# Performance work log

Hardware: AMD Instinct MI355X
Metric: run time of the kernel (lower is better)

## Reference

```python
import jax, jax.numpy as jnp
import numpy as np

N = 100_000      # nodes
E = 1_600_000    # edges (before self loops)
F_IN = 128       # dataset.num_node_features
H = 64           # hidden_channels
C = 10           # dataset.num_classes
B = 128          # graphs in batch
NEG_SLOPE = 0.2  # GATConv default


def setup_inputs() -> dict:
    key = jax.random.key(0)
    ks = jax.random.split(key, 16)
    s = 0.05
    x = jax.random.normal(ks[0], (N, F_IN), jnp.float32)
    edge_index = jax.random.randint(ks[1], (2, E), 0, N, dtype=jnp.int32).astype(jnp.int64)
    batch = jnp.sort(jax.random.randint(ks[2], (N,), 0, B, dtype=jnp.int32)).astype(jnp.int64)
    inp = {"x": x, "edge_index": edge_index, "batch": batch}
    # GATConv params: lin weight [out,in], att_src/att_dst [out], bias [out]
    dims = [(H, F_IN), (H, H), (H, H)]
    for i, (o, fi) in enumerate(dims, start=1):
        k = jax.random.split(ks[2 + i], 4)
        inp[f"W{i}"] = jax.random.normal(k[0], (o, fi), jnp.float32) * s
        inp[f"a_src{i}"] = jax.random.normal(k[1], (o,), jnp.float32) * s
        inp[f"a_dst{i}"] = jax.random.normal(k[2], (o,), jnp.float32) * s
        inp[f"b{i}"] = jax.random.normal(k[3], (o,), jnp.float32) * s
    inp["W_lin"] = jax.random.normal(ks[8], (C, H), jnp.float32) * s
    inp["b_lin"] = jax.random.normal(ks[9], (C,), jnp.float32) * s
    return inp


def gat_conv(x, src, dst, W, a_src, a_dst, b):
    # x: [N,Fin]; src/dst: [E+N] (self loops appended)
    h = x @ W.T                      # [N,H]
    e_src = h @ a_src                # [N] per-node src score
    e_dst = h @ a_dst                # [N] per-node dst score
    e = jax.nn.leaky_relu(e_src[src] + e_dst[dst], NEG_SLOPE)  # [E+N]
    # segment softmax over incoming edges of each dst node
    m = jax.ops.segment_max(e, dst, num_segments=N)
    ex = jnp.exp(e - m[dst])
    denom = jax.ops.segment_sum(ex, dst, num_segments=N)
    alpha = ex / denom[dst]          # [E+N]
    out = jax.ops.segment_sum(h[src] * alpha[:, None], dst, num_segments=N)
    return out + b


def reference(x, edge_index, batch, W1, a_src1, a_dst1, b1,
              W2, a_src2, a_dst2, b2, W3, a_src3, a_dst3, b3,
              W_lin, b_lin):
    loops = jnp.arange(N, dtype=edge_index.dtype)
    src = jnp.concatenate([edge_index[0], loops])
    dst = jnp.concatenate([edge_index[1], loops])
    h = jax.nn.relu(gat_conv(x, src, dst, W1, a_src1, a_dst1, b1))
    h = jax.nn.relu(gat_conv(h, src, dst, W2, a_src2, a_dst2, b2))
    h = gat_conv(h, src, dst, W3, a_src3, a_dst3, b3)
    # global mean pool over graphs
    sums = jax.ops.segment_sum(h, batch, num_segments=B)          # [B,H]
    cnt = jax.ops.segment_sum(jnp.ones((N,), h.dtype), batch, num_segments=B)
    pooled = sums / jnp.maximum(cnt, 1.0)[:, None]
    # dropout is identity in eval mode
    return pooled @ W_lin.T + b_lin   # [B,C]
```

## Files before the change

kernel.cpp:

```cpp
#include <hip/hip_runtime.h>
#include <hip/hip_bf16.h>

#define NN 100000
#define EE 1600000
#define ETOT 1700000
#define FIN1 128
#define HD 64
#define NC 10
#define NB 128
#define NEG 0.2f
#define LOG2E 1.44269504f

#define NBKT 196
#define BCAP 10240
#define BLKE 4096


static constexpr size_t OFF_HA   = 0;
static constexpr size_t OFF_HB   = (size_t)NN * HD;
static constexpr size_t OFF_ESA  = (size_t)NN * HD * 2;
static constexpr size_t OFF_EDA  = OFF_ESA + (size_t)NN * 4;
static constexpr size_t OFF_ESB  = OFF_EDA + (size_t)NN * 4;
static constexpr size_t OFF_EDB  = OFF_ESB + (size_t)NN * 4;
static constexpr size_t OFF_ROW  = OFF_EDB + (size_t)NN * 4;
static constexpr size_t OFF_CSR  = OFF_ROW + (size_t)(NN + 4) * 4;
static constexpr size_t OFF_GC   = OFF_CSR + (size_t)ETOT * 4;
static constexpr size_t OFF_POOL = OFF_GC + 1024;

typedef __attribute__((ext_vector_type(8))) short short8;
typedef __attribute__((ext_vector_type(4))) float floatx4;
typedef __attribute__((ext_vector_type(2))) float floatx2;

__device__ __forceinline__ unsigned short f2bf(float f) {
  unsigned u = __float_as_uint(f);
  if ((u & 0x7F800000u) == 0x7F800000u) return (unsigned short)(u >> 16);
  return (unsigned short)((u + 0x7FFFu + ((u >> 16) & 1u)) >> 16);
}
__device__ __forceinline__ unsigned pk2(float a, float b) {
  return (unsigned)f2bf(a) | ((unsigned)f2bf(b) << 16);
}

#if __has_builtin(__builtin_amdgcn_cvt_pk_fp8_f32) && __has_builtin(__builtin_amdgcn_cvt_pk_f32_fp8)
#define HW_FP8 1
#endif
__device__ __forceinline__ unsigned enc1_fp8(float f) {
  _Float16 hf = (_Float16)f;
  unsigned short b = __builtin_bit_cast(unsigned short, hf);
  unsigned s = ((unsigned)b >> 8) & 0x80u;
  int mag = b & 0x7fff;
  if (mag < 0x2380) return s;
  int r = mag + 0x3F + ((mag >> 7) & 1);
  int m = (r >> 7) - 64;
  if (m > 0x7E) m = 0x7E;
  return s | (unsigned)m;
}
__device__ __forceinline__ unsigned pack4_fp8(float a, float b, float c, float d) {
#ifdef HW_FP8
  int w = __builtin_amdgcn_cvt_pk_fp8_f32(a, b, 0, false);
  w = __builtin_amdgcn_cvt_pk_fp8_f32(c, d, w, true);
  return (unsigned)w;
#else
  return enc1_fp8(a) | (enc1_fp8(b) << 8) | (enc1_fp8(c) << 16) | (enc1_fp8(d) << 24);
#endif
}
__device__ __forceinline__ float dec1_fp8(unsigned byte) {
  unsigned short hb = (unsigned short)(((byte & 0x80u) << 8) | ((byte & 0x7fu) << 7));
  _Float16 hf = __builtin_bit_cast(_Float16, hb);
  return (float)hf * 256.0f;
}
template <bool HI>
__device__ __forceinline__ floatx2 unpk2_fp8(unsigned w) {
#ifdef HW_FP8
  return __builtin_amdgcn_cvt_pk_f32_fp8((int)w, HI);
#else
  unsigned s = HI ? (w >> 16) : w;
  floatx2 r; r.x = dec1_fp8(s & 0xffu); r.y = dec1_fp8((s >> 8) & 0xffu);
  return r;
#endif
}

__global__ __launch_bounds__(256) void bucketA_kernel(
    const int* __restrict__ EI, unsigned* __restrict__ bucketed,
    int* __restrict__ gcur) {
  __shared__ int cnt[NBKT];
  __shared__ int base[NBKT];
  const int t = threadIdx.x;
  const long long start = (long long)blockIdx.x * BLKE;
  unsigned pk[BLKE / 256];
  short bk[BLKE / 256];
  for (int i = t; i < NBKT; i += 256) cnt[i] = 0;
  __syncthreads();
#pragma unroll
  for (int j = 0; j < BLKE / 256; j++) {
    long long k = start + t + 256 * j;
    bk[j] = -1;
    if (k < ETOT) {
      int s, d;
      if (k < EE) { s = EI[k]; d = EI[(long long)EE + k]; }
      else        { s = d = (int)(k - EE); }
      int b = d >> 9;
      pk[j] = ((unsigned)s << 9) | (unsigned)(d & 511);
      bk[j] = (short)b;
      atomicAdd(&cnt[b], 1);
    }
  }
  __syncthreads();
  if (t < NBKT) {
    base[t] = (cnt[t] > 0) ? atomicAdd(&gcur[t], cnt[t]) : 0;
    cnt[t] = 0;
  }
  __syncthreads();
#pragma unroll
  for (int j = 0; j < BLKE / 256; j++) {
    if (bk[j] >= 0) {
      int b = bk[j];
      int pos = base[b] + atomicAdd(&cnt[b], 1);
      if (pos < BCAP) bucketed[(long long)b * BCAP + pos] = pk[j];
    }
  }
}

__global__ __launch_bounds__(256) void bucketB_kernel(
    const unsigned* __restrict__ bucketed, const int* __restrict__ gcur,
    int* __restrict__ rowptr, int* __restrict__ csr) {
  __shared__ int sc[256];
  __shared__ int hist[512];
  __shared__ int cur[512];
  __shared__ int ssum[256];
  const int t = threadIdx.x;
  const int b = blockIdx.x;
  int gv = (t < NBKT) ? gcur[t] : 0;
  sc[t] = gv;
  __syncthreads();
  for (int off = 1; off < 256; off <<= 1) {
    int add = (t >= off) ? sc[t - off] : 0;
    __syncthreads();
    sc[t] += add;
    __syncthreads();
  }
  const int cnt = gcur[b];
  const int base = sc[b] - cnt;
  if (b == 0 && t == 0) rowptr[NN] = ETOT;
  const unsigned* bp = bucketed + (long long)b * BCAP;
  hist[t] = 0; hist[t + 256] = 0;
  __syncthreads();
  for (int i = t; i < cnt; i += 256) atomicAdd(&hist[bp[i] & 511], 1);
  __syncthreads();
  int a0 = hist[2 * t], a1 = hist[2 * t + 1];
  int s = a0 + a1;
  ssum[t] = s;
  __syncthreads();
  for (int off = 1; off < 256; off <<= 1) {
    int add = (t >= off) ? ssum[t - off] : 0;
    __syncthreads();
    ssum[t] += add;
    __syncthreads();
  }
  int ex = ssum[t] - s;
  cur[2 * t] = ex;
  cur[2 * t + 1] = ex + a0;
  int gn = b * 512 + 2 * t;
  if (gn < NN) rowptr[gn] = base + ex;
  if (gn + 1 < NN) rowptr[gn + 1] = base + ex + a0;
  __syncthreads();
  for (int i = t; i < cnt; i += 256) {
    unsigned e = bp[i];
    int pos = atomicAdd(&cur[e & 511], 1);
    csr[base + pos] = (int)(e >> 9);
  }
}

__global__ __launch_bounds__(256) void gemm1_kernel(
    const float* __restrict__ X, const float* __restrict__ W,
    const float* __restrict__ As, const float* __restrict__ Ad,
    unsigned* __restrict__ hout, float* __restrict__ es, float* __restrict__ ed) {
  constexpr int K = FIN1, RW = K / 2;
  __shared__ unsigned Xw[64 * RW];
  __shared__ unsigned Ww[64 * RW];
  const int t = threadIdx.x;
  const int nodeBase = blockIdx.x * 64;

  for (int i4 = t * 4; i4 < 64 * K; i4 += 1024) {
    int node = i4 >> 7, k = i4 & (K - 1);
    float4 v = make_float4(0.f, 0.f, 0.f, 0.f);
    if (nodeBase + node < NN)
      v = *(const float4*)(X + ((long long)(nodeBase + node) << 7) + k);
    uint2 p = make_uint2(pk2(v.x, v.y), pk2(v.z, v.w));
    int kw = k >> 1;
    *(uint2*)&Xw[node * RW + (kw ^ ((node & 7) << 2))] = p;
  }
  for (int i4 = t * 4; i4 < 64 * K; i4 += 1024) {
    int f = i4 >> 7, k = i4 & (K - 1);
    float4 v = *(const float4*)(W + ((long long)f << 7) + k);
    uint2 p = make_uint2(pk2(v.x, v.y), pk2(v.z, v.w));
    int kw = k >> 1;
    *(uint2*)&Ww[f * RW + (kw ^ ((f & 7) << 2))] = p;
  }
  __syncthreads();

  const int w = t >> 6, l = t & 63, m = l & 15, q = l >> 4;
  const int nodeLoc = 16 * w + m;
  const int sxa = (nodeLoc & 7) << 2;
  floatx4 acc[4];
#pragma unroll
  for (int nt = 0; nt < 4; nt++) acc[nt] = (floatx4){0.f, 0.f, 0.f, 0.f};
#pragma unroll
  for (int kc = 0; kc < K; kc += 32) {
    const int kcw = (kc >> 1) + 4 * q;
    short8 af = *(const short8*)&Xw[nodeLoc * RW + (kcw ^ sxa)];
#pragma unroll
    for (int nt = 0; nt < 4; nt++) {
      int f = 16 * nt + m;
      short8 bf = *(const short8*)&Ww[f * RW + (kcw ^ ((f & 7) << 2))];
      acc[nt] = __builtin_amdgcn_mfma_f32_16x16x32_bf16(af, bf, acc[nt], 0, 0, 0);
    }
  }
  float asv[4], adv[4];
#pragma unroll
  for (int nt = 0; nt < 4; nt++) { asv[nt] = As[16 * nt + m]; adv[nt] = Ad[16 * nt + m]; }
#pragma unroll
  for (int r = 0; r < 4; r++) {
    float ss = 0.f, sd2 = 0.f;
#pragma unroll
    for (int nt = 0; nt < 4; nt++) {
      ss = fmaf(acc[nt][r], asv[nt], ss);
      sd2 = fmaf(acc[nt][r], adv[nt], sd2);
    }
#pragma unroll
    for (int off = 1; off < 16; off <<= 1) {
      ss += __shfl_xor(ss, off);
      sd2 += __shfl_xor(sd2, off);
    }
    if (m == 0) {
      int gn = nodeBase + 16 * w + 4 * q + r;
      if (gn < NN) { es[gn] = ss * LOG2E; ed[gn] = sd2 * LOG2E; }
    }
  }
  {
    int gn = nodeBase + 16 * w + 4 * q;
#pragma unroll
    for (int nt = 0; nt < 4; nt++) {
#pragma unroll
      for (int r = 0; r < 4; r++) {
        float v = acc[nt][r];
        float p1 = __shfl_xor(v, 1);
        float p2 = __shfl_xor(v, 2);
        float p3 = __shfl_xor(v, 3);
        if ((m & 3) == 0 && (gn + r) < NN)
          hout[(gn + r) * 16 + 4 * nt + (m >> 2)] = pack4_fp8(v, p1, p2, p3);
      }
    }
  }
}

__global__ __launch_bounds__(256) void agg_gemm_kernel(
    const int* __restrict__ rowptr, const int* __restrict__ csr,
    const float* __restrict__ esIn, const float* __restrict__ edIn,
    const uint2* __restrict__ h8In, const float* __restrict__ biasA,
    const float* __restrict__ W, const float* __restrict__ As,
    const float* __restrict__ Ad,
    unsigned* __restrict__ hOut, float* __restrict__ esOut, float* __restrict__ edOut) {
  constexpr int K = HD, RW = K / 2;
  __shared__ unsigned Xw[64 * RW];
  __shared__ unsigned Ww[64 * RW];
  const int t = threadIdx.x;
  const int nodeBase = blockIdx.x * 64;

  for (int i4 = t * 4; i4 < 64 * K; i4 += 1024) {
    int f = i4 >> 6, k = i4 & (K - 1);
    float4 v = *(const float4*)(W + ((long long)f << 6) + k);
    uint2 p = make_uint2(pk2(v.x, v.y), pk2(v.z, v.w));
    int kw = k >> 1;
    *(uint2*)&Ww[f * RW + (kw ^ ((f & 7) << 2))] = p;
  }

  const int fl = t & 7;
#pragma unroll
  for (int half = 0; half < 2; half++) {
    const int nl = half * 32 + (t >> 3);
    const int n = nodeBase + nl;
    const int sxa = (nl & 7) << 2;
    const int kwb = (4 * fl) ^ sxa;
    if (n < NN) {
      const float edn = edIn[n];
      const int row = rowptr[n];
      const int end = rowptr[n + 1];
      const int endm1 = end - 1;
      float den = 0.f;
      float acc[8];
#pragma unroll
      for (int j = 0; j < 8; j++) acc[j] = 0.f;
      for (int i = row; i < end; i += 4) {
        int k1 = i + 1, k2 = i + 2, k3 = i + 3;
        k1 = (k1 < end) ? k1 : endm1;
        k2 = (k2 < end) ? k2 : endm1;
        k3 = (k3 < end) ? k3 : endm1;
        int s0 = csr[i], s1 = csr[k1], s2 = csr[k2], s3 = csr[k3];
        uint2 u0 = h8In[s0 * 8 + fl];
        uint2 u1 = h8In[s1 * 8 + fl];
        uint2 u2 = h8In[s2 * 8 + fl];
        uint2 u3 = h8In[s3 * 8 + fl];
        float e0 = esIn[s0] + edn, e1 = esIn[s1] + edn;
        float e2 = esIn[s2] + edn, e3 = esIn[s3] + edn;
        e0 = fmaxf(e0, NEG * e0);
        e1 = fmaxf(e1, NEG * e1);
        e2 = fmaxf(e2, NEG * e2);
        e3 = fmaxf(e3, NEG * e3);
        float w0 = exp2f(e0), w1 = exp2f(e1), w2 = exp2f(e2), w3 = exp2f(e3);
        w1 = (i + 1 < end) ? w1 : 0.f;
        w2 = (i + 2 < end) ? w2 : 0.f;
        w3 = (i + 3 < end) ? w3 : 0.f;
        den += (w0 + w1) + (w2 + w3);
#define ACC_E(w, u)                                            \
        { floatx2 fA = unpk2_fp8<false>((u).x);                \
          floatx2 fB = unpk2_fp8<true>((u).x);                 \
          floatx2 fC = unpk2_fp8<false>((u).y);                \
          floatx2 fD = unpk2_fp8<true>((u).y);                 \
          acc[0] = fmaf(w, fA.x, acc[0]); acc[1] = fmaf(w, fA.y, acc[1]); \
          acc[2] = fmaf(w, fB.x, acc[2]); acc[3] = fmaf(w, fB.y, acc[3]); \
          acc[4] = fmaf(w, fC.x, acc[4]); acc[5] = fmaf(w, fC.y, acc[5]); \
          acc[6] = fmaf(w, fD.x, acc[6]); acc[7] = fmaf(w, fD.y, acc[7]); }
        ACC_E(w0, u0) ACC_E(w1, u1) ACC_E(w2, u2) ACC_E(w3, u3)
#undef ACC_E
      }
      const float inv = 1.0f / den;
      float v[8];
#pragma unroll
      for (int j = 0; j < 8; j++)
        v[j] = fmaxf(acc[j] * inv + biasA[8 * fl + j], 0.f);
      *(uint2*)&Xw[nl * RW + kwb] = make_uint2(pk2(v[0], v[1]), pk2(v[2], v[3]));
      *(uint2*)&Xw[nl * RW + kwb + 2] = make_uint2(pk2(v[4], v[5]), pk2(v[6], v[7]));
    } else {
      *(uint2*)&Xw[nl * RW + kwb] = make_uint2(0u, 0u);
      *(uint2*)&Xw[nl * RW + kwb + 2] = make_uint2(0u, 0u);
    }
  }
  __syncthreads();

  const int w = t >> 6, l = t & 63, m = l & 15, q = l >> 4;
  const int nodeLoc = 16 * w + m;
  const int sxa = (nodeLoc & 7) << 2;
  floatx4 acc[4];
#pragma unroll
  for (int nt = 0; nt < 4; nt++) acc[nt] = (floatx4){0.f, 0.f, 0.f, 0.f};
#pragma unroll
  for (int kc = 0; kc < K; kc += 32) {
    const int kcw = (kc >> 1) + 4 * q;
    short8 af = *(const short8*)&Xw[nodeLoc * RW + (kcw ^ sxa)];
#pragma unroll
    for (int nt = 0; nt < 4; nt++) {
      int f = 16 * nt + m;
      short8 bf = *(const short8*)&Ww[f * RW + (kcw ^ ((f & 7) << 2))];
      acc[nt] = __builtin_amdgcn_mfma_f32_16x16x32_bf16(af, bf, acc[nt], 0, 0, 0);
    }
  }
  float asv[4], adv[4];
#pragma unroll
  for (int nt = 0; nt < 4; nt++) { asv[nt] = As[16 * nt + m]; adv[nt] = Ad[16 * nt + m]; }
#pragma unroll
  for (int r = 0; r < 4; r++) {
    float ss = 0.f, sd2 = 0.f;
#pragma unroll
    for (int nt = 0; nt < 4; nt++) {
      ss = fmaf(acc[nt][r], asv[nt], ss);
      sd2 = fmaf(acc[nt][r], adv[nt], sd2);
    }
#pragma unroll
    for (int off = 1; off < 16; off <<= 1) {
      ss += __shfl_xor(ss, off);
      sd2 += __shfl_xor(sd2, off);
    }
    if (m == 0) {
      int gn = nodeBase + 16 * w + 4 * q + r;
      if (gn < NN) { esOut[gn] = ss * LOG2E; edOut[gn] = sd2 * LOG2E; }
    }
  }
  {
    int gn = nodeBase + 16 * w + 4 * q;
#pragma unroll
    for (int nt = 0; nt < 4; nt++) {
#pragma unroll
      for (int r = 0; r < 4; r++) {
        float v = acc[nt][r];
        float p1 = __shfl_xor(v, 1);
        float p2 = __shfl_xor(v, 2);
        float p3 = __shfl_xor(v, 3);
        if ((m & 3) == 0 && (gn + r) < NN)
          hOut[(gn + r) * 16 + 4 * nt + (m >> 2)] = pack4_fp8(v, p1, p2, p3);
      }
    }
  }
}

__global__ __launch_bounds__(256) void agg3_pool_kernel(
    const int* __restrict__ rowptr, const int* __restrict__ csr,
    const float* __restrict__ esIn, const float* __restrict__ edIn,
    const uint2* __restrict__ h8In, const float* __restrict__ biasA,
    const int* __restrict__ batch, float* __restrict__ pooled) {
  __shared__ float P[32 * 66];
  __shared__ int gl[32];
  const int t = threadIdx.x;
  const int fl = t & 7;
  const int nl = t >> 3;
  const int n = blockIdx.x * 32 + nl;
  if (t < 32) gl[t] = batch[blockIdx.x * 32 + t];
  {
    const float edn = edIn[n];
    const int row = rowptr[n];
    const int end = rowptr[n + 1];
    const int endm1 = end - 1;
    float den = 0.f;
    float acc[8];
#pragma unroll
    for (int j = 0; j < 8; j++) acc[j] = 0.f;
    for (int i = row; i < end; i += 4) {
      int k1 = i + 1, k2 = i + 2, k3 = i + 3;
      k1 = (k1 < end) ? k1 : endm1;
      k2 = (k2 < end) ? k2 : endm1;
      k3 = (k3 < end) ? k3 : endm1;
      int s0 = csr[i], s1 = csr[k1], s2 = csr[k2], s3 = csr[k3];
      uint2 u0 = h8In[s0 * 8 + fl];
      uint2 u1 = h8In[s1 * 8 + fl];
      uint2 u2 = h8In[s2 * 8 + fl];
      uint2 u3 = h8In[s3 * 8 + fl];
      float e0 = esIn[s0] + edn, e1 = esIn[s1] + edn;
      float e2 = esIn[s2] + edn, e3 = esIn[s3] + edn;
      e0 = fmaxf(e0, NEG * e0);
      e1 = fmaxf(e1, NEG * e1);
      e2 = fmaxf(e2, NEG * e2);
      e3 = fmaxf(e3, NEG * e3);
      float w0 = exp2f(e0), w1 = exp2f(e1), w2 = exp2f(e2), w3 = exp2f(e3);
      w1 = (i + 1 < end) ? w1 : 0.f;
      w2 = (i + 2 < end) ? w2 : 0.f;
      w3 = (i + 3 < end) ? w3 : 0.f;
      den += (w0 + w1) + (w2 + w3);
#define ACC_E(w, u)                                            \
      { floatx2 fA = unpk2_fp8<false>((u).x);                  \
        floatx2 fB = unpk2_fp8<true>((u).x);                   \
        floatx2 fC = unpk2_fp8<false>((u).y);                  \
        floatx2 fD = unpk2_fp8<true>((u).y);                   \
        acc[0] = fmaf(w, fA.x, acc[0]); acc[1] = fmaf(w, fA.y, acc[1]); \
        acc[2] = fmaf(w, fB.x, acc[2]); acc[3] = fmaf(w, fB.y, acc[3]); \
        acc[4] = fmaf(w, fC.x, acc[4]); acc[5] = fmaf(w, fC.y, acc[5]); \
        acc[6] = fmaf(w, fD.x, acc[6]); acc[7] = fmaf(w, fD.y, acc[7]); }
      ACC_E(w0, u0) ACC_E(w1, u1) ACC_E(w2, u2) ACC_E(w3, u3)
#undef ACC_E
    }
    const float inv = 1.0f / den;
#pragma unroll
    for (int j = 0; j < 8; j++)
      P[nl * 66 + 8 * fl + j] = acc[j] * inv + biasA[8 * fl + j];
  }
  __syncthreads();
  if (t < HD) {
    const int f = t;
    float s = 0.f;
    int gcur = gl[0];
    for (int k = 0; k < 32; k++) {
      int g = gl[k];
      if (g != gcur) {
        atomicAdd(&pooled[gcur * HD + f], s);
        s = 0.f;
        gcur = g;
      }
      s += P[k * 66 + f];
    }
    atomicAdd(&pooled[gcur * HD + f], s);
  }
}

__device__ __forceinline__ int lower_bound_batch(const int* bt, int target) {
  int lo = 0, hi = NN;
  while (lo < hi) {
    int mid = (lo + hi) >> 1;
    if (bt[mid] < target) lo = mid + 1; else hi = mid;
  }
  return lo;
}

__global__ void final_kernel(
    const float* __restrict__ pooled, const int* __restrict__ batch,
    const float* __restrict__ Wlin, const float* __restrict__ blin,
    float* __restrict__ out) {
  int t = blockIdx.x * blockDim.x + threadIdx.x;
  if (t >= NB * NC) return;
  int b = t / NC, c = t - b * NC;
  int lo = lower_bound_batch(batch, b);
  int hi = lower_bound_batch(batch, b + 1);
  float inv = 1.0f / fmaxf((float)(hi - lo), 1.0f);
  float a = blin[c];
#pragma unroll 16
  for (int f = 0; f < HD; f++)
    a = fmaf(pooled[b * HD + f] * inv, Wlin[(long long)c * HD + f], a);
  out[t] = a;
}

extern "C" void kernel_launch(void* const* d_in, const int* in_sizes, int n_in,
                              void* d_out, int out_size, void* d_ws, size_t ws_size,
                              hipStream_t stream) {
  char* ws = (char*)d_ws;
  unsigned* hA        = (unsigned*)(ws + OFF_HA);
  unsigned* hB        = (unsigned*)(ws + OFF_HB);
  unsigned* bucketed  = (unsigned*)(ws + OFF_HA);
  float*    esA      = (float*)(ws + OFF_ESA);
  float*    edA      = (float*)(ws + OFF_EDA);
  float*    esB      = (float*)(ws + OFF_ESB);
  float*    edB      = (float*)(ws + OFF_EDB);
  int*      rowptr   = (int*)(ws + OFF_ROW);
  int*      csr      = (int*)(ws + OFF_CSR);
  int*      gcur     = (int*)(ws + OFF_GC);
  float*    pooled   = (float*)(ws + OFF_POOL);

  const float* X  = (const float*)d_in[0];
  const int*   EI = (const int*)d_in[1];
  const int*   BT = (const int*)d_in[2];
  const float* Wm[3] = {(const float*)d_in[3], (const float*)d_in[7], (const float*)d_in[11]};
  const float* As[3] = {(const float*)d_in[4], (const float*)d_in[8], (const float*)d_in[12]};
  const float* Ad[3] = {(const float*)d_in[5], (const float*)d_in[9], (const float*)d_in[13]};
  const float* Bb[3] = {(const float*)d_in[6], (const float*)d_in[10], (const float*)d_in[14]};
  const float* Wl = (const float*)d_in[15];
  const float* bl = (const float*)d_in[16];

  (void)hipMemsetAsync(gcur, 0, 1024 + (size_t)NB * HD * 4, stream);
  bucketA_kernel<<<(ETOT + BLKE - 1) / BLKE, 256, 0, stream>>>(EI, bucketed, gcur);
  bucketB_kernel<<<NBKT, 256, 0, stream>>>(bucketed, gcur, rowptr, csr);

  const int gblocks = (NN + 63) / 64;
  gemm1_kernel<<<gblocks, 256, 0, stream>>>(X, Wm[0], As[0], Ad[0], hA, esA, edA);
  agg_gemm_kernel<<<gblocks, 256, 0, stream>>>(
      rowptr, csr, esA, edA, (const uint2*)hA, Bb[0],
      Wm[1], As[1], Ad[1], hB, esB, edB);
  agg_gemm_kernel<<<gblocks, 256, 0, stream>>>(
      rowptr, csr, esB, edB, (const uint2*)hB, Bb[1],
      Wm[2], As[2], Ad[2], hA, esA, edA);
  agg3_pool_kernel<<<NN / 32, 256, 0, stream>>>(
      rowptr, csr, esA, edA, (const uint2*)hA, Bb[2], BT, pooled);
  final_kernel<<<(NB * NC + 255) / 256, 256, 0, stream>>>(pooled, BT, Wl, bl, (float*)d_out);
}
```

Measured before the change: 299.6 us.

## Merge edge bucketing and first-layer GEMM into one heterogeneous launch

Edge-bucketing blocks and layer-1 GEMM blocks now run in a single kernel, with the block index deciding which role each block takes. The independent work can overlap on the GPU, and one launch plus its serialization gap goes away. Because the bucket buffer previously aliased the hA output, it gets its own workspace region so the two roles do not conflict. The cost is a larger workspace and a shared 32KB LDS allocation, which may lower occupancy for the bucketing blocks.

```diff
diff --git a/kernel.cpp b/kernel.cpp
--- a/kernel.cpp
+++ b/kernel.cpp
@@ -14,6 +14,8 @@
 #define NBKT 196
 #define BCAP 10240
 #define BLKE 4096
+#define ABLOCKS ((ETOT + BLKE - 1) / BLKE)
+#define GBLOCKS ((NN + 63) / 64)
 
 
 static constexpr size_t OFF_HA   = 0;
@@ -26,6 +28,7 @@
 static constexpr size_t OFF_CSR  = OFF_ROW + (size_t)(NN + 4) * 4;
 static constexpr size_t OFF_GC   = OFF_CSR + (size_t)ETOT * 4;
 static constexpr size_t OFF_POOL = OFF_GC + 1024;
+static constexpr size_t OFF_BKT  = OFF_POOL + (size_t)NB * HD * 4;
 
 typedef __attribute__((ext_vector_type(8))) short short8;
 typedef __attribute__((ext_vector_type(4))) float floatx4;
@@ -79,13 +82,13 @@
 #endif
 }
 
-__global__ __launch_bounds__(256) void bucketA_kernel(
-    const int* __restrict__ EI, unsigned* __restrict__ bucketed,
-    int* __restrict__ gcur) {
-  __shared__ int cnt[NBKT];
-  __shared__ int base[NBKT];
+__device__ __forceinline__ void bucketA_body(
+    int bid, const int* __restrict__ EI, unsigned* __restrict__ bucketed,
+    int* __restrict__ gcur, char* smem) {
+  int* cnt = (int*)smem;
+  int* base = cnt + NBKT;
   const int t = threadIdx.x;
-  const long long start = (long long)blockIdx.x * BLKE;
+  const long long start = (long long)bid * BLKE;
   unsigned pk[BLKE / 256];
   short bk[BLKE / 256];
   for (int i = t; i < NBKT; i += 256) cnt[i] = 0;
@@ -120,6 +123,102 @@
   }
 }
 
+__device__ __forceinline__ void gemm1_body(
+    int bid, const float* __restrict__ X, const float* __restrict__ W,
+    const float* __restrict__ As, const float* __restrict__ Ad,
+    unsigned* __restrict__ hout, float* __restrict__ es, float* __restrict__ ed,
+    char* smem) {
+  constexpr int K = FIN1, RW = K / 2;
+  unsigned* Xw = (unsigned*)smem;
+  unsigned* Ww = (unsigned*)(smem + 16384);
+  const int t = threadIdx.x;
+  const int nodeBase = bid * 64;
+
+  for (int i4 = t * 4; i4 < 64 * K; i4 += 1024) {
+    int node = i4 >> 7, k = i4 & (K - 1);
+    float4 v = make_float4(0.f, 0.f, 0.f, 0.f);
+    if (nodeBase + node < NN)
+      v = *(const float4*)(X + ((long long)(nodeBase + node) << 7) + k);
+    uint2 p = make_uint2(pk2(v.x, v.y), pk2(v.z, v.w));
+    int kw = k >> 1;
+    *(uint2*)&Xw[node * RW + (kw ^ ((node & 7) << 2))] = p;
+  }
+  for (int i4 = t * 4; i4 < 64 * K; i4 += 1024) {
+    int f = i4 >> 7, k = i4 & (K - 1);
+    float4 v = *(const float4*)(W + ((long long)f << 7) + k);
+    uint2 p = make_uint2(pk2(v.x, v.y), pk2(v.z, v.w));
+    int kw = k >> 1;
+    *(uint2*)&Ww[f * RW + (kw ^ ((f & 7) << 2))] = p;
+  }
+  __syncthreads();
+
+  const int w = t >> 6, l = t & 63, m = l & 15, q = l >> 4;
+  const int nodeLoc = 16 * w + m;
+  const int sxa = (nodeLoc & 7) << 2;
+  floatx4 acc[4];
+#pragma unroll
+  for (int nt = 0; nt < 4; nt++) acc[nt] = (floatx4){0.f, 0.f, 0.f, 0.f};
+#pragma unroll
+  for (int kc = 0; kc < K; kc += 32) {
+    const int kcw = (kc >> 1) + 4 * q;
+    short8 af = *(const short8*)&Xw[nodeLoc * RW + (kcw ^ sxa)];
+#pragma unroll
+    for (int nt = 0; nt < 4; nt++) {
+      int f = 16 * nt + m;
+      short8 bf = *(const short8*)&Ww[f * RW + (kcw ^ ((f & 7) << 2))];
+      acc[nt] = __builtin_amdgcn_mfma_f32_16x16x32_bf16(af, bf, acc[nt], 0, 0, 0);
+    }
+  }
+  float asv[4], adv[4];
+#pragma unroll
+  for (int nt = 0; nt < 4; nt++) { asv[nt] = As[16 * nt + m]; adv[nt] = Ad[16 * nt + m]; }
+#pragma unroll
+  for (int r = 0; r < 4; r++) {
+    float ss = 0.f, sd2 = 0.f;
+#pragma unroll
+    for (int nt = 0; nt < 4; nt++) {
+      ss = fmaf(acc[nt][r], asv[nt], ss);
+      sd2 = fmaf(acc[nt][r], adv[nt], sd2);
+    }
+#pragma unroll
+    for (int off = 1; off < 16; off <<= 1) {
+      ss += __shfl_xor(ss, off);
+      sd2 += __shfl_xor(sd2, off);
+    }
+    if (m == 0) {
+      int gn = nodeBase + 16 * w + 4 * q + r;
+      if (gn < NN) { es[gn] = ss * LOG2E; ed[gn] = sd2 * LOG2E; }
+    }
+  }
+  {
+    int gn = nodeBase + 16 * w + 4 * q;
+#pragma unroll
+    for (int nt = 0; nt < 4; nt++) {
+#pragma unroll
+      for (int r = 0; r < 4; r++) {
+        float v = acc[nt][r];
+        float p1 = __shfl_xor(v, 1);
+        float p2 = __shfl_xor(v, 2);
+        float p3 = __shfl_xor(v, 3);
+        if ((m & 3) == 0 && (gn + r) < NN)
+          hout[(gn + r) * 16 + 4 * nt + (m >> 2)] = pack4_fp8(v, p1, p2, p3);
+      }
+    }
+  }
+}
+
+__global__ __launch_bounds__(256) void buildA_gemm1_kernel(
+    const int* __restrict__ EI, unsigned* __restrict__ bucketed, int* __restrict__ gcur,
+    const float* __restrict__ X, const float* __restrict__ W,
+    const float* __restrict__ As, const float* __restrict__ Ad,
+    unsigned* __restrict__ hout, float* __restrict__ es, float* __restrict__ ed) {
+  __shared__ __align__(16) char smem[32768];
+  if (blockIdx.x < ABLOCKS)
+    bucketA_body(blockIdx.x, EI, bucketed, gcur, smem);
+  else
+    gemm1_body(blockIdx.x - ABLOCKS, X, W, As, Ad, hout, es, ed, smem);
+}
+
 __global__ __launch_bounds__(256) void bucketB_kernel(
     const unsigned* __restrict__ bucketed, const int* __restrict__ gcur,
     int* __restrict__ rowptr, int* __restrict__ csr) {
@@ -167,89 +266,6 @@
     unsigned e = bp[i];
     int pos = atomicAdd(&cur[e & 511], 1);
     csr[base + pos] = (int)(e >> 9);
-  }
-}
-
-__global__ __launch_bounds__(256) void gemm1_kernel(
-    const float* __restrict__ X, const float* __restrict__ W,
-    const float* __restrict__ As, const float* __restrict__ Ad,
-    unsigned* __restrict__ hout, float* __restrict__ es, float* __restrict__ ed) {
-  constexpr int K = FIN1, RW = K / 2;
-  __shared__ unsigned Xw[64 * RW];
-  __shared__ unsigned Ww[64 * RW];
-  const int t = threadIdx.x;
-  const int nodeBase = blockIdx.x * 64;
-
-  for (int i4 = t * 4; i4 < 64 * K; i4 += 1024) {
-    int node = i4 >> 7, k = i4 & (K - 1);
-    float4 v = make_float4(0.f, 0.f, 0.f, 0.f);
-    if (nodeBase + node < NN)
-      v = *(const float4*)(X + ((long long)(nodeBase + node) << 7) + k);
-    uint2 p = make_uint2(pk2(v.x, v.y), pk2(v.z, v.w));
-    int kw = k >> 1;
-    *(uint2*)&Xw[node * RW + (kw ^ ((node & 7) << 2))] = p;
-  }
-  for (int i4 = t * 4; i4 < 64 * K; i4 += 1024) {
-    int f = i4 >> 7, k = i4 & (K - 1);
-    float4 v = *(const float4*)(W + ((long long)f << 7) + k);
-    uint2 p = make_uint2(pk2(v.x, v.y), pk2(v.z, v.w));
-    int kw = k >> 1;
-    *(uint2*)&Ww[f * RW + (kw ^ ((f & 7) << 2))] = p;
-  }
-  __syncthreads();
-
-  const int w = t >> 6, l = t & 63, m = l & 15, q = l >> 4;
-  const int nodeLoc = 16 * w + m;
-  const int sxa = (nodeLoc & 7) << 2;
-  floatx4 acc[4];
-#pragma unroll
-  for (int nt = 0; nt < 4; nt++) acc[nt] = (floatx4){0.f, 0.f, 0.f, 0.f};
-#pragma unroll
-  for (int kc = 0; kc < K; kc += 32) {
-    const int kcw = (kc >> 1) + 4 * q;
-    short8 af = *(const short8*)&Xw[nodeLoc * RW + (kcw ^ sxa)];
-#pragma unroll
-    for (int nt = 0; nt < 4; nt++) {
-      int f = 16 * nt + m;
-      short8 bf = *(const short8*)&Ww[f * RW + (kcw ^ ((f & 7) << 2))];
-      acc[nt] = __builtin_amdgcn_mfma_f32_16x16x32_bf16(af, bf, acc[nt], 0, 0, 0);
-    }
-  }
-  float asv[4], adv[4];
-#pragma unroll
-  for (int nt = 0; nt < 4; nt++) { asv[nt] = As[16 * nt + m]; adv[nt] = Ad[16 * nt + m]; }
-#pragma unroll
-  for (int r = 0; r < 4; r++) {
-    float ss = 0.f, sd2 = 0.f;
-#pragma unroll
-    for (int nt = 0; nt < 4; nt++) {
-      ss = fmaf(acc[nt][r], asv[nt], ss);
-      sd2 = fmaf(acc[nt][r], adv[nt], sd2);
-    }
-#pragma unroll
-    for (int off = 1; off < 16; off <<= 1) {
-      ss += __shfl_xor(ss, off);
-      sd2 += __shfl_xor(sd2, off);
-    }
-    if (m == 0) {
-      int gn = nodeBase + 16 * w + 4 * q + r;
-      if (gn < NN) { es[gn] = ss * LOG2E; ed[gn] = sd2 * LOG2E; }
-    }
-  }
-  {
-    int gn = nodeBase + 16 * w + 4 * q;
-#pragma unroll
-    for (int nt = 0; nt < 4; nt++) {
-#pragma unroll
-      for (int r = 0; r < 4; r++) {
-        float v = acc[nt][r];
-        float p1 = __shfl_xor(v, 1);
-        float p2 = __shfl_xor(v, 2);
-        float p3 = __shfl_xor(v, 3);
-        if ((m & 3) == 0 && (gn + r) < NN)
-          hout[(gn + r) * 16 + 4 * nt + (m >> 2)] = pack4_fp8(v, p1, p2, p3);
-      }
-    }
   }
 }
 
@@ -499,9 +515,8 @@
                               void* d_out, int out_size, void* d_ws, size_t ws_size,
                               hipStream_t stream) {
   char* ws = (char*)d_ws;
-  unsigned* hA        = (unsigned*)(ws + OFF_HA);
-  unsigned* hB        = (unsigned*)(ws + OFF_HB);
-  unsigned* bucketed  = (unsigned*)(ws + OFF_HA);
+  unsigned* hA       = (unsigned*)(ws + OFF_HA);
+  unsigned* hB       = (unsigned*)(ws + OFF_HB);
   float*    esA      = (float*)(ws + OFF_ESA);
   float*    edA      = (float*)(ws + OFF_EDA);
   float*    esB      = (float*)(ws + OFF_ESB);
@@ -510,6 +525,7 @@
   int*      csr      = (int*)(ws + OFF_CSR);
   int*      gcur     = (int*)(ws + OFF_GC);
   float*    pooled   = (float*)(ws + OFF_POOL);
+  unsigned* bucketed = (unsigned*)(ws + OFF_BKT);
 
   const float* X  = (const float*)d_in[0];
   const int*   EI = (const int*)d_in[1];
@@ -522,15 +538,13 @@
   const float* bl = (const float*)d_in[16];
 
   (void)hipMemsetAsync(gcur, 0, 1024 + (size_t)NB * HD * 4, stream);
-  bucketA_kernel<<<(ETOT + BLKE - 1) / BLKE, 256, 0, stream>>>(EI, bucketed, gcur);
+  buildA_gemm1_kernel<<<ABLOCKS + GBLOCKS, 256, 0, stream>>>(
+      EI, bucketed, gcur, X, Wm[0], As[0], Ad[0], hA, esA, edA);
   bucketB_kernel<<<NBKT, 256, 0, stream>>>(bucketed, gcur, rowptr, csr);
-
-  const int gblocks = (NN + 63) / 64;
-  gemm1_kernel<<<gblocks, 256, 0, stream>>>(X, Wm[0], As[0], Ad[0], hA, esA, edA);
-  agg_gemm_kernel<<<gblocks, 256, 0, stream>>>(
+  agg_gemm_kernel<<<GBLOCKS, 256, 0, stream>>>(
       rowptr, csr, esA, edA, (const uint2*)hA, Bb[0],
       Wm[1], As[1], Ad[1], hB, esB, edB);
-  agg_gemm_kernel<<<gblocks, 256, 0, stream>>>(
+  agg_gemm_kernel<<<GBLOCKS, 256, 0, stream>>>(
       rowptr, csr, esB, edB, (const uint2*)hB, Bb[1],
       Wm[2], As[2], Ad[2], hA, esA, edA);
   agg3_pool_kernel<<<NN / 32, 256, 0, stream>>>(
```

New measurement: 295.1 us. About the same (-1.5%).
